# Kernel optimization log

Hardware: AMD Instinct MI355X
Metric: run time of the kernel (lower is better)

The kernel has to match this reference:

```python
import jax, jax.numpy as jnp
import numpy as np

# MSDeformAttn dims inferred from Linear shapes: 8 heads * 4 levels * 2 points
H, L, P, D, C = 8, 4, 2, 32, 256
SHAPES = [(128, 128), (64, 64), (32, 32), (16, 16)]  # (H_l, W_l) per level
NV = sum(h * w for h, w in SHAPES)  # 21760
STARTS = np.cumsum([0] + [h * w for h, w in SHAPES])


def _bilinear(val, lx, ly, Hl, Wl):
    """grid_sample(align_corners=False, padding='zeros') equivalent.
    val: [B, H, Hl*Wl, D]; lx, ly: [B, H, N] normalized sample coords in [0,1].
    Returns [B, H, N, D]."""
    x = lx * Wl - 0.5
    y = ly * Hl - 0.5
    x0 = jnp.floor(x)
    y0 = jnp.floor(y)
    fx = x - x0
    fy = y - y0
    x0i = x0.astype(jnp.int32)
    y0i = y0.astype(jnp.int32)
    out = jnp.zeros(val.shape[:2] + (x.shape[-1], val.shape[-1]), val.dtype)
    corners = ((0, 0, (1 - fx) * (1 - fy)), (1, 0, fx * (1 - fy)),
               (0, 1, (1 - fx) * fy), (1, 1, fx * fy))
    for dx, dy, w in corners:
        xi = x0i + dx
        yi = y0i + dy
        valid = ((xi >= 0) & (xi < Wl) & (yi >= 0) & (yi < Hl)).astype(val.dtype)
        idx = jnp.clip(yi, 0, Hl - 1) * Wl + jnp.clip(xi, 0, Wl - 1)
        g = jnp.take_along_axis(val, idx[..., None], axis=2)  # [B,H,N,D]
        out = out + g * (w * valid)[..., None]
    return out


def setup_inputs() -> dict:
    key = jax.random.key(0)
    ks = jax.random.split(key, 8)
    B, NQ = 4, 1000
    s = 0.02
    return {
        "query": jax.random.normal(ks[0], (B, NQ, C), jnp.float32),
        "value": jax.random.normal(ks[1], (B, NV, C), jnp.float32),
        "reference_points": jax.random.uniform(ks[2], (B, NQ, L, 2), jnp.float32),
        "W_off": jax.random.normal(ks[3], (C, H * L * P * 2), jnp.float32) * s,
        "b_off": jnp.zeros((H * L * P * 2,), jnp.float32),
        "W_attn": jax.random.normal(ks[4], (C, H * L * P), jnp.float32) * s,
        "b_attn": jnp.zeros((H * L * P,), jnp.float32),
        "W_val": jax.random.normal(ks[5], (C, C), jnp.float32) * s,
        "b_val": jnp.zeros((C,), jnp.float32),
        "W_out": jax.random.normal(ks[6], (C, C), jnp.float32) * s,
        "b_out": jnp.zeros((C,), jnp.float32),
    }


def reference(query, value, reference_points, W_off, b_off, W_attn, b_attn,
              W_val, b_val, W_out, b_out):
    B, NQ, _ = query.shape
    # value projection -> per-head values [B, H, NV, D]
    v = (value @ W_val + b_val).reshape(B, NV, H, D).transpose(0, 2, 1, 3)
    # sampling offsets [B, NQ, H, L, P, 2]
    off = (query @ W_off + b_off).reshape(B, NQ, H, L, P, 2)
    # attention weights: softmax over L*P
    attn = jax.nn.softmax((query @ W_attn + b_attn).reshape(B, NQ, H, L * P), axis=-1)
    attn = attn.reshape(B, NQ, H, L, P)
    # normalizer (W_l, H_l) per level, matching Deformable-DETR
    wh = jnp.asarray([[w, h] for h, w in SHAPES], dtype=query.dtype)  # [L,2]
    loc = reference_points[:, :, None, :, None, :] + off / wh[None, None, None, :, None, :]
    out = jnp.zeros((B, H, NQ, D), dtype=query.dtype)
    for l, (hl, wl) in enumerate(SHAPES):
        vl = v[:, :, STARTS[l]:STARTS[l + 1], :]                 # [B,H,hl*wl,D]
        lx = loc[:, :, :, l, :, 0].transpose(0, 2, 1, 3).reshape(B, H, NQ * P)
        ly = loc[:, :, :, l, :, 1].transpose(0, 2, 1, 3).reshape(B, H, NQ * P)
        s = _bilinear(vl, lx, ly, hl, wl).reshape(B, H, NQ, P, D)
        al = attn[:, :, :, l, :].transpose(0, 2, 1, 3)           # [B,H,NQ,P]
        out = out + jnp.sum(s * al[..., None], axis=3)
    out = out.transpose(0, 2, 1, 3).reshape(B, NQ, C)
    return out @ W_out + b_out  # dropout(p=0) is identity
```

## Files before the change

kernel.cpp:

```cpp
#include <hip/hip_runtime.h>

#define HH 8
#define LL 4
#define PP 2
#define DD 32
#define CC 256
#define NVV 21760
#define NQQ 1000
#define BB 4
#define NQT (BB * NQQ)

typedef __attribute__((ext_vector_type(8))) short short8;
typedef __attribute__((ext_vector_type(4))) short shortv4;
typedef __attribute__((ext_vector_type(4))) float f32x4;

__device__ __forceinline__ unsigned short f2bf(float f) {
    unsigned u = __float_as_uint(f);
    u += 0x7FFF + ((u >> 16) & 1);
    return (unsigned short)(u >> 16);
}
__device__ __forceinline__ float bf2f(unsigned short h) {
    return __uint_as_float(((unsigned)h) << 16);
}

__device__ __forceinline__ void gload_lds16(const void* g, void* l) {
    __builtin_amdgcn_global_load_lds(
        (const __attribute__((address_space(1))) unsigned int*)g,
        (__attribute__((address_space(3))) unsigned int*)l, 16, 0, 0);
}

__global__ __launch_bounds__(256) void prep_kernel(
    const float* __restrict__ Wv, const float* __restrict__ Woff,
    const float* __restrict__ Wattn, const float* __restrict__ Wout,
    unsigned short* __restrict__ Wslc, unsigned short* __restrict__ W1T,
    unsigned short* __restrict__ WoT)
{
    const int c = blockIdx.x;
    const int n = threadIdx.x;
    Wslc[(c >> 5) * 8192 + n * 32 + (c & 31)] = f2bf(Wv[c * CC + n]);
    if (n < 192) {
        float x = (n < 128) ? Woff[c * 128 + n] : Wattn[c * 64 + (n - 128)];
        W1T[n * CC + c] = f2bf(x);
    }
    WoT[n * CC + c] = f2bf(Wout[c * CC + n]);
}

__global__ __launch_bounds__(512) void valproj_mfma(
    const float* __restrict__ value, const unsigned short* __restrict__ Wslc,
    const float* __restrict__ bv, unsigned short* __restrict__ v_out)
{
    __shared__ __align__(16) unsigned short Bs[8][256][32];

    const int tid = threadIdx.x;
    const int w = tid >> 6;
    const int lane = tid & 63;
    const int lr = lane & 15;
    const int q = lane >> 4;
    const int bm = blockIdx.x * 128;
    const int b = bm / NVV;

#pragma unroll
    for (int i = 0; i < 16; ++i) {
        size_t off = (size_t)i * 8192 + (size_t)tid * 16;
        gload_lds16((const char*)Wslc + off, (char*)&Bs[0][0][0] + off);
    }
    __syncthreads();

    const float* arow = value + (size_t)(bm + w * 16 + lr) * CC;
    float4 a0[8], a1[8];
#pragma unroll
    for (int s = 0; s < 8; ++s) {
        const float* p = arow + s * 32 + q * 8;
        a0[s] = *(const float4*)p;
        a1[s] = *(const float4*)(p + 4);
    }

    f32x4 acc[16] = {};
#pragma unroll
    for (int s = 0; s < 8; ++s) {
        short8 af;
        af[0] = (short)f2bf(a0[s].x); af[1] = (short)f2bf(a0[s].y);
        af[2] = (short)f2bf(a0[s].z); af[3] = (short)f2bf(a0[s].w);
        af[4] = (short)f2bf(a1[s].x); af[5] = (short)f2bf(a1[s].y);
        af[6] = (short)f2bf(a1[s].z); af[7] = (short)f2bf(a1[s].w);
#pragma unroll
        for (int nf = 0; nf < 16; ++nf) {
            short8 bf = *(const short8*)&Bs[s][nf * 16 + lr][q * 8];
            acc[nf] = __builtin_amdgcn_mfma_f32_16x16x32_bf16(af, bf, acc[nf],
                                                              0, 0, 0);
        }
    }

#pragma unroll
    for (int nf = 0; nf < 16; ++nf) {
        int col = nf * 16 + lr;
        int h = col >> 5, d = col & 31;
        float bias = bv[col];
        int n0 = bm - b * NVV + w * 16 + q * 4;
        size_t obase = (size_t)((b * HH + h) * NVV + n0) * DD + d;
#pragma unroll
        for (int r = 0; r < 4; ++r)
            v_out[obase + (size_t)r * DD] = f2bf(acc[nf][r] + bias);
    }
}

__global__ __launch_bounds__(256) void logits_mfma(
    const float* __restrict__ query, const unsigned short* __restrict__ W1T,
    const float* __restrict__ b_off, const float* __restrict__ b_attn,
    float* __restrict__ logits)
{
    __shared__ unsigned short As[32][72];
    __shared__ unsigned short Bs[192][72];
    const int tid = threadIdx.x;
    const int lane = tid & 63;
    const int wave = tid >> 6;
    const int bm = blockIdx.x * 32;
    const int lr = lane & 15;
    const int q = lane >> 4;
    f32x4 acc[2][3] = {};

    for (int k0 = 0; k0 < CC; k0 += 64) {
        float4 a[2];
        short8 wv[6];
#pragma unroll
        for (int i = 0; i < 2; ++i) {
            int u = tid + 256 * i;
            a[i] = *(const float4*)&query[(size_t)(bm + (u >> 4)) * CC + k0 +
                                          (u & 15) * 4];
        }
#pragma unroll
        for (int i = 0; i < 6; ++i) {
            int u = tid + 256 * i;
            wv[i] = *(const short8*)&W1T[(size_t)(u >> 3) * CC + k0 + (u & 7) * 8];
        }
        __syncthreads();
#pragma unroll
        for (int i = 0; i < 2; ++i) {
            int u = tid + 256 * i;
            shortv4 p;
            p[0] = (short)f2bf(a[i].x); p[1] = (short)f2bf(a[i].y);
            p[2] = (short)f2bf(a[i].z); p[3] = (short)f2bf(a[i].w);
            *(shortv4*)&As[u >> 4][(u & 15) * 4] = p;
        }
#pragma unroll
        for (int i = 0; i < 6; ++i) {
            int u = tid + 256 * i;
            *(short8*)&Bs[u >> 3][(u & 7) * 8] = wv[i];
        }
        __syncthreads();

#pragma unroll
        for (int kk = 0; kk < 2; ++kk) {
            short8 afr[2], bfr[3];
#pragma unroll
            for (int mf = 0; mf < 2; ++mf)
                afr[mf] = *(const short8*)&As[mf * 16 + lr][kk * 32 + q * 8];
#pragma unroll
            for (int nf = 0; nf < 3; ++nf)
                bfr[nf] =
                    *(const short8*)&Bs[wave * 48 + nf * 16 + lr][kk * 32 + q * 8];
#pragma unroll
            for (int mf = 0; mf < 2; ++mf)
#pragma unroll
                for (int nf = 0; nf < 3; ++nf)
                    acc[mf][nf] = __builtin_amdgcn_mfma_f32_16x16x32_bf16(
                        afr[mf], bfr[nf], acc[mf][nf], 0, 0, 0);
        }
        __syncthreads();
    }

#pragma unroll
    for (int nf = 0; nf < 3; ++nf) {
        int col = wave * 48 + nf * 16 + lr;
        float bias = (col < 128) ? b_off[col] : b_attn[col - 128];
#pragma unroll
        for (int mf = 0; mf < 2; ++mf)
#pragma unroll
            for (int r = 0; r < 4; ++r) {
                int m = bm + mf * 16 + q * 4 + r;
                logits[(size_t)m * 192 + col] = acc[mf][nf][r] + bias;
            }
    }
}

__global__ __launch_bounds__(256) void sample_kernel(
    const float* __restrict__ logits,
    const float* __restrict__ refp,
    const unsigned short* __restrict__ v,
    unsigned short* __restrict__ mid)
{
    __shared__ float offl[128];
    __shared__ float attnl[64];
    __shared__ float refl[8];

    const int qy = blockIdx.x;
    const int b = qy / NQQ;
    const int tid = threadIdx.x;

    if (tid < 192) {
        float t = logits[(size_t)qy * 192 + tid];
        if (tid < 128) offl[tid] = t;
        else attnl[tid - 128] = t;
    } else if (tid < 200) {
        refl[tid - 192] = refp[(size_t)qy * 8 + (tid - 192)];
    }
    __syncthreads();

    if (tid < 8) {
        float m = -1e30f;
#pragma unroll
        for (int j = 0; j < 8; ++j) m = fmaxf(m, attnl[tid * 8 + j]);
        float s = 0.f, e[8];
#pragma unroll
        for (int j = 0; j < 8; ++j) {
            e[j] = __expf(attnl[tid * 8 + j] - m);
            s += e[j];
        }
        float inv = 1.f / s;
#pragma unroll
        for (int j = 0; j < 8; ++j) attnl[tid * 8 + j] = e[j] * inv;
    }
    __syncthreads();

    const int h = tid >> 5, d = tid & 31;
    const unsigned short* vh = v + (size_t)(b * HH + h) * NVV * DD;
    const int starts[4] = {0, 16384, 20480, 21504};
    const float szs[4] = {128.f, 64.f, 32.f, 16.f};

    float acc = 0.f;
#pragma unroll
    for (int l = 0; l < LL; ++l) {
        const float S = szs[l];
        const int Wl = (int)S;
        const float refx = refl[l * 2 + 0];
        const float refy = refl[l * 2 + 1];
        const unsigned short* vl = vh + (size_t)starts[l] * DD;
#pragma unroll
        for (int p = 0; p < PP; ++p) {
            const int oi = h * 16 + l * 4 + p * 2;
            float lx = refx + offl[oi + 0] / S;
            float ly = refy + offl[oi + 1] / S;
            float x = lx * S - 0.5f;
            float y = ly * S - 0.5f;
            float x0f = floorf(x), y0f = floorf(y);
            float fx = x - x0f, fy = y - y0f;
            int x0 = (int)x0f, y0 = (int)y0f;
            float a = attnl[h * 8 + l * 2 + p];
            float sacc = 0.f;
#pragma unroll
            for (int dy = 0; dy < 2; ++dy) {
#pragma unroll
                for (int dx = 0; dx < 2; ++dx) {
                    int xi = x0 + dx, yi = y0 + dy;
                    float wgt = (dx ? fx : 1.f - fx) * (dy ? fy : 1.f - fy);
                    bool valid = (xi >= 0) && (xi < Wl) && (yi >= 0) && (yi < Wl);
                    int xc = min(max(xi, 0), Wl - 1);
                    int yc = min(max(yi, 0), Wl - 1);
                    float g = bf2f(vl[(size_t)(yc * Wl + xc) * DD + d]);
                    sacc += g * (valid ? wgt : 0.f);
                }
            }
            acc += a * sacc;
        }
    }
    mid[(size_t)qy * CC + h * 32 + d] = f2bf(acc);
}

__global__ __launch_bounds__(256) void out_mfma(
    const unsigned short* __restrict__ mid,
    const unsigned short* __restrict__ WoT, const float* __restrict__ b_out,
    float* __restrict__ out)
{
    __shared__ unsigned short As[32][72];
    __shared__ unsigned short Bs[256][72];
    const int tid = threadIdx.x;
    const int lane = tid & 63;
    const int wave = tid >> 6;
    const int bm = blockIdx.x * 32;
    const int lr = lane & 15;
    const int q = lane >> 4;
    f32x4 acc[2][4] = {};

    for (int k0 = 0; k0 < CC; k0 += 64) {
        short8 a0 = *(const short8*)&mid[(size_t)(bm + (tid >> 3)) * CC + k0 +
                                         (tid & 7) * 8];
        short8 wv[8];
#pragma unroll
        for (int i = 0; i < 8; ++i) {
            int u = tid + 256 * i;
            wv[i] = *(const short8*)&WoT[(size_t)(u >> 3) * CC + k0 + (u & 7) * 8];
        }
        __syncthreads();
        *(short8*)&As[tid >> 3][(tid & 7) * 8] = a0;
#pragma unroll
        for (int i = 0; i < 8; ++i) {
            int u = tid + 256 * i;
            *(short8*)&Bs[u >> 3][(u & 7) * 8] = wv[i];
        }
        __syncthreads();

#pragma unroll
        for (int kk = 0; kk < 2; ++kk) {
            short8 afr[2], bfr[4];
#pragma unroll
            for (int mf = 0; mf < 2; ++mf)
                afr[mf] = *(const short8*)&As[mf * 16 + lr][kk * 32 + q * 8];
#pragma unroll
            for (int nf = 0; nf < 4; ++nf)
                bfr[nf] =
                    *(const short8*)&Bs[wave * 64 + nf * 16 + lr][kk * 32 + q * 8];
#pragma unroll
            for (int mf = 0; mf < 2; ++mf)
#pragma unroll
                for (int nf = 0; nf < 4; ++nf)
                    acc[mf][nf] = __builtin_amdgcn_mfma_f32_16x16x32_bf16(
                        afr[mf], bfr[nf], acc[mf][nf], 0, 0, 0);
        }
        __syncthreads();
    }

#pragma unroll
    for (int nf = 0; nf < 4; ++nf) {
        int col = wave * 64 + nf * 16 + lr;
        float bias = b_out[col];
#pragma unroll
        for (int mf = 0; mf < 2; ++mf)
#pragma unroll
            for (int r = 0; r < 4; ++r) {
                int m = bm + mf * 16 + q * 4 + r;
                out[(size_t)m * CC + col] = acc[mf][nf][r] + bias;
            }
    }
}

extern "C" void kernel_launch(void* const* d_in, const int* in_sizes, int n_in,
                              void* d_out, int out_size, void* d_ws, size_t ws_size,
                              hipStream_t stream) {
    const float* query  = (const float*)d_in[0];
    const float* value  = (const float*)d_in[1];
    const float* refp   = (const float*)d_in[2];
    const float* W_off  = (const float*)d_in[3];
    const float* b_off  = (const float*)d_in[4];
    const float* W_attn = (const float*)d_in[5];
    const float* b_attn = (const float*)d_in[6];
    const float* W_val  = (const float*)d_in[7];
    const float* b_val  = (const float*)d_in[8];
    const float* W_out  = (const float*)d_in[9];
    const float* b_out  = (const float*)d_in[10];
    float* out = (float*)d_out;

    char* ws = (char*)d_ws;
    unsigned short* Wslc   = (unsigned short*)(ws);
    unsigned short* v_ws   = (unsigned short*)(ws + 131072);
    unsigned short* W1T    = (unsigned short*)(ws + 44695552);
    unsigned short* WoT    = (unsigned short*)(ws + 44793856);
    float*          logits = (float*)(ws + 44924928);
    unsigned short* mid    = (unsigned short*)(ws + 47996928);

    prep_kernel<<<CC, 256, 0, stream>>>(W_val, W_off, W_attn, W_out,
                                        Wslc, W1T, WoT);
    valproj_mfma<<<(BB * NVV) / 128, 512, 0, stream>>>(value, Wslc, b_val, v_ws);
    logits_mfma<<<NQT / 32, 256, 0, stream>>>(query, W1T, b_off, b_attn, logits);
    sample_kernel<<<NQT, 256, 0, stream>>>(logits, refp, v_ws, mid);
    out_mfma<<<NQT / 32, 256, 0, stream>>>(mid, WoT, b_out, out);
}
```

Measured before the change: 68.15 us.

## Retile value projection into N-halves with swizzled LDS and coalesced row-major output

The value-projection GEMM is split into two N-halves per 128-row tile, with twice as many blocks, and uses a 2x2 wave layout. An XOR swizzle on the weight LDS layout avoids bank conflicts, A-tile loads are double-buffered, and the bf16 packing uses the hardware cvt_pk instruction. The output is staged through LDS and written row-major [B,NV,256] with 16-byte stores instead of scattered per-head 2-byte writes. The sampling kernel is changed to index this new layout, so each bilinear corner gather now strides 512 bytes per texel rather than 64.

```diff
diff --git a/kernel.cpp b/kernel.cpp
--- a/kernel.cpp
+++ b/kernel.cpp
@@ -22,6 +22,11 @@
 __device__ __forceinline__ float bf2f(unsigned short h) {
     return __uint_as_float(((unsigned)h) << 16);
 }
+__device__ __forceinline__ unsigned cvtpk(float lo, float hi) {
+    unsigned r;
+    asm volatile("v_cvt_pk_bf16_f32 %0, %1, %2" : "=v"(r) : "v"(lo), "v"(hi));
+    return r;
+}
 
 __device__ __forceinline__ void gload_lds16(const void* g, void* l) {
     __builtin_amdgcn_global_load_lds(
@@ -37,7 +42,12 @@
 {
     const int c = blockIdx.x;
     const int n = threadIdx.x;
-    Wslc[(c >> 5) * 8192 + n * 32 + (c & 31)] = f2bf(Wv[c * CC + n]);
+    {
+        int half = n >> 7, n7 = n & 127, s = c >> 5, kk = c & 31;
+        unsigned addr = n7 * 64 + kk * 2;
+        addr ^= ((n7 & 3) << 4);
+        Wslc[half * 32768 + s * 4096 + (addr >> 1)] = f2bf(Wv[c * CC + n]);
+    }
     if (n < 192) {
         float x = (n < 128) ? Woff[c * 128 + n] : Wattn[c * 64 + (n - 128)];
         W1T[n * CC + c] = f2bf(x);
@@ -45,62 +55,97 @@
     WoT[n * CC + c] = f2bf(Wout[c * CC + n]);
 }
 
-__global__ __launch_bounds__(512) void valproj_mfma(
+__global__ __launch_bounds__(512, 4) void valproj_mfma(
     const float* __restrict__ value, const unsigned short* __restrict__ Wslc,
     const float* __restrict__ bv, unsigned short* __restrict__ v_out)
 {
-    __shared__ __align__(16) unsigned short Bs[8][256][32];
+    __shared__ __align__(16) unsigned short Bs[32768];
 
     const int tid = threadIdx.x;
     const int w = tid >> 6;
     const int lane = tid & 63;
+    const int wm = w >> 1;
+    const int wn = w & 1;
     const int lr = lane & 15;
     const int q = lane >> 4;
-    const int bm = blockIdx.x * 128;
-    const int b = bm / NVV;
-
-#pragma unroll
-    for (int i = 0; i < 16; ++i) {
+    const int mt = blockIdx.x >> 1;
+    const int hf = blockIdx.x & 1;
+    const int bm = mt * 128;
+
+#pragma unroll
+    for (int i = 0; i < 8; ++i) {
         size_t off = (size_t)i * 8192 + (size_t)tid * 16;
-        gload_lds16((const char*)Wslc + off, (char*)&Bs[0][0][0] + off);
+        gload_lds16((const char*)Wslc + (size_t)hf * 65536 + off,
+                    (char*)&Bs[0] + off);
     }
     __syncthreads();
 
-    const float* arow = value + (size_t)(bm + w * 16 + lr) * CC;
-    float4 a0[8], a1[8];
+    const float* arow0 = value + (size_t)(bm + wm * 32 + lr) * CC;
+
+    float4 ab[2][2][2];
+#define LOADA(p, s)                                                          \
+    {                                                                        \
+        _Pragma("unroll") for (int mf = 0; mf < 2; ++mf) {                   \
+            const float* pp = arow0 + mf * 16 * CC + (s) * 32 + q * 8;       \
+            ab[p][mf][0] = *(const float4*)pp;                               \
+            ab[p][mf][1] = *(const float4*)(pp + 4);                         \
+        }                                                                    \
+    }
+
+    LOADA(0, 0);
+    LOADA(1, 1);
+
+    f32x4 acc[2][4] = {};
 #pragma unroll
     for (int s = 0; s < 8; ++s) {
-        const float* p = arow + s * 32 + q * 8;
-        a0[s] = *(const float4*)p;
-        a1[s] = *(const float4*)(p + 4);
-    }
-
-    f32x4 acc[16] = {};
-#pragma unroll
-    for (int s = 0; s < 8; ++s) {
-        short8 af;
-        af[0] = (short)f2bf(a0[s].x); af[1] = (short)f2bf(a0[s].y);
-        af[2] = (short)f2bf(a0[s].z); af[3] = (short)f2bf(a0[s].w);
-        af[4] = (short)f2bf(a1[s].x); af[5] = (short)f2bf(a1[s].y);
-        af[6] = (short)f2bf(a1[s].z); af[7] = (short)f2bf(a1[s].w);
-#pragma unroll
-        for (int nf = 0; nf < 16; ++nf) {
-            short8 bf = *(const short8*)&Bs[s][nf * 16 + lr][q * 8];
-            acc[nf] = __builtin_amdgcn_mfma_f32_16x16x32_bf16(af, bf, acc[nf],
-                                                              0, 0, 0);
-        }
-    }
-
-#pragma unroll
-    for (int nf = 0; nf < 16; ++nf) {
-        int col = nf * 16 + lr;
-        int h = col >> 5, d = col & 31;
-        float bias = bv[col];
-        int n0 = bm - b * NVV + w * 16 + q * 4;
-        size_t obase = (size_t)((b * HH + h) * NVV + n0) * DD + d;
-#pragma unroll
-        for (int r = 0; r < 4; ++r)
-            v_out[obase + (size_t)r * DD] = f2bf(acc[nf][r] + bias);
+        const int cur = s & 1;
+        short8 af[2];
+#pragma unroll
+        for (int mf = 0; mf < 2; ++mf) {
+            float4 f0 = ab[cur][mf][0], f1 = ab[cur][mf][1];
+            uint4 uv = {cvtpk(f0.x, f0.y), cvtpk(f0.z, f0.w),
+                        cvtpk(f1.x, f1.y), cvtpk(f1.z, f1.w)};
+            af[mf] = __builtin_bit_cast(short8, uv);
+        }
+        if (s < 6) LOADA(cur, s + 2);
+        short8 bfr[4];
+#pragma unroll
+        for (int nf = 0; nf < 4; ++nf) {
+            int idx = s * 4096 +
+                      (((wn * 64 + nf * 16 + lr) * 32 + q * 8) ^ ((lr & 3) << 3));
+            bfr[nf] = *(const short8*)&Bs[idx];
+        }
+#pragma unroll
+        for (int mf = 0; mf < 2; ++mf)
+#pragma unroll
+            for (int nf = 0; nf < 4; ++nf)
+                acc[mf][nf] = __builtin_amdgcn_mfma_f32_16x16x32_bf16(
+                    af[mf], bfr[nf], acc[mf][nf], 0, 0, 0);
+    }
+#undef LOADA
+
+    __syncthreads();
+#pragma unroll
+    for (int nf = 0; nf < 4; ++nf) {
+        int col = wn * 64 + nf * 16 + lr;
+        float bias = bv[hf * 128 + col];
+#pragma unroll
+        for (int mf = 0; mf < 2; ++mf)
+#pragma unroll
+            for (int r = 0; r < 4; ++r) {
+                int row = wm * 32 + mf * 16 + q * 4 + r;
+                Bs[row * 136 + col] = f2bf(acc[mf][nf][r] + bias);
+            }
+    }
+    __syncthreads();
+    {
+        int row = tid >> 2, ch = tid & 3;
+        size_t obase = (size_t)(bm + row) * 256 + hf * 128 + ch * 32;
+#pragma unroll
+        for (int i = 0; i < 4; ++i) {
+            short8 val = *(const short8*)&Bs[row * 136 + ch * 32 + i * 8];
+            *(short8*)&v_out[obase + i * 8] = val;
+        }
     }
 }
 
@@ -110,7 +155,7 @@
     float* __restrict__ logits)
 {
     __shared__ unsigned short As[32][72];
-    __shared__ unsigned short Bs[192][72];
+    __shared__ unsigned short Bsl[192][72];
     const int tid = threadIdx.x;
     const int lane = tid & 63;
     const int wave = tid >> 6;
@@ -145,7 +190,7 @@
 #pragma unroll
         for (int i = 0; i < 6; ++i) {
             int u = tid + 256 * i;
-            *(short8*)&Bs[u >> 3][(u & 7) * 8] = wv[i];
+            *(short8*)&Bsl[u >> 3][(u & 7) * 8] = wv[i];
         }
         __syncthreads();
 
@@ -158,7 +203,7 @@
 #pragma unroll
             for (int nf = 0; nf < 3; ++nf)
                 bfr[nf] =
-                    *(const short8*)&Bs[wave * 48 + nf * 16 + lr][kk * 32 + q * 8];
+                    *(const short8*)&Bsl[wave * 48 + nf * 16 + lr][kk * 32 + q * 8];
 #pragma unroll
             for (int mf = 0; mf < 2; ++mf)
 #pragma unroll
@@ -223,7 +268,6 @@
     __syncthreads();
 
     const int h = tid >> 5, d = tid & 31;
-    const unsigned short* vh = v + (size_t)(b * HH + h) * NVV * DD;
     const int starts[4] = {0, 16384, 20480, 21504};
     const float szs[4] = {128.f, 64.f, 32.f, 16.f};
 
@@ -234,7 +278,8 @@
         const int Wl = (int)S;
         const float refx = refl[l * 2 + 0];
         const float refy = refl[l * 2 + 1];
-        const unsigned short* vl = vh + (size_t)starts[l] * DD;
+        const unsigned short* vl =
+            v + (size_t)(b * NVV + starts[l]) * 256 + h * 32 + d;
 #pragma unroll
         for (int p = 0; p < PP; ++p) {
             const int oi = h * 16 + l * 4 + p * 2;
@@ -256,7 +301,7 @@
                     bool valid = (xi >= 0) && (xi < Wl) && (yi >= 0) && (yi < Wl);
                     int xc = min(max(xi, 0), Wl - 1);
                     int yc = min(max(yi, 0), Wl - 1);
-                    float g = bf2f(vl[(size_t)(yc * Wl + xc) * DD + d]);
+                    float g = bf2f(vl[(size_t)(yc * Wl + xc) * 256]);
                     sacc += g * (valid ? wgt : 0.f);
                 }
             }
@@ -272,7 +317,7 @@
     float* __restrict__ out)
 {
     __shared__ unsigned short As[32][72];
-    __shared__ unsigned short Bs[256][72];
+    __shared__ unsigned short Bso[256][72];
     const int tid = threadIdx.x;
     const int lane = tid & 63;
     const int wave = tid >> 6;
@@ -295,7 +340,7 @@
 #pragma unroll
         for (int i = 0; i < 8; ++i) {
             int u = tid + 256 * i;
-            *(short8*)&Bs[u >> 3][(u & 7) * 8] = wv[i];
+            *(short8*)&Bso[u >> 3][(u & 7) * 8] = wv[i];
         }
         __syncthreads();
 
@@ -308,7 +353,7 @@
 #pragma unroll
             for (int nf = 0; nf < 4; ++nf)
                 bfr[nf] =
-                    *(const short8*)&Bs[wave * 64 + nf * 16 + lr][kk * 32 + q * 8];
+                    *(const short8*)&Bso[wave * 64 + nf * 16 + lr][kk * 32 + q * 8];
 #pragma unroll
             for (int mf = 0; mf < 2; ++mf)
 #pragma unroll
@@ -359,7 +404,8 @@
 
     prep_kernel<<<CC, 256, 0, stream>>>(W_val, W_off, W_attn, W_out,
                                         Wslc, W1T, WoT);
-    valproj_mfma<<<(BB * NVV) / 128, 512, 0, stream>>>(value, Wslc, b_val, v_ws);
+    valproj_mfma<<<(BB * NVV) / 128 * 2, 512, 0, stream>>>(value, Wslc, b_val,
+                                                           v_ws);
     logits_mfma<<<NQT / 32, 256, 0, stream>>>(query, W1T, b_off, b_attn, logits);
     sample_kernel<<<NQT, 256, 0, stream>>>(logits, refp, v_ws, mid);
     out_mfma<<<NQT / 32, 256, 0, stream>>>(mid, WoT, b_out, out);
```

Result: slower. 95.36 us (+39.9%).

## Reorder value projection after sampling to skip full value-map projection

Applied to the files above, without the earlier changes.

Drops the projection of the whole value map (87k rows x 256 x 256). Since bilinear sampling and attention weighting are linear, it instead samples the raw fp32 value rows, aggregates them per query and head, and then applies the per-head slice of W_val to that aggregate, adding the bias scaled by the summed corner weights. This removes a large GEMM and its bf16 intermediate write. In exchange each sample gathers full 256-wide fp32 rows instead of 32-wide bf16 head slices, and each block runs a scalar, non-MFMA per-query projection from LDS.

```diff
diff --git a/kernel.cpp b/kernel.cpp
--- a/kernel.cpp
+++ b/kernel.cpp
@@ -9,6 +9,7 @@
 #define NQQ 1000
 #define BB 4
 #define NQT (BB * NQQ)
+#define QB 4
 
 typedef __attribute__((ext_vector_type(8))) short short8;
 typedef __attribute__((ext_vector_type(4))) short shortv4;
@@ -23,85 +24,20 @@
     return __uint_as_float(((unsigned)h) << 16);
 }
 
-__device__ __forceinline__ void gload_lds16(const void* g, void* l) {
-    __builtin_amdgcn_global_load_lds(
-        (const __attribute__((address_space(1))) unsigned int*)g,
-        (__attribute__((address_space(3))) unsigned int*)l, 16, 0, 0);
-}
-
 __global__ __launch_bounds__(256) void prep_kernel(
     const float* __restrict__ Wv, const float* __restrict__ Woff,
     const float* __restrict__ Wattn, const float* __restrict__ Wout,
-    unsigned short* __restrict__ Wslc, unsigned short* __restrict__ W1T,
+    unsigned short* __restrict__ WT, unsigned short* __restrict__ W1T,
     unsigned short* __restrict__ WoT)
 {
     const int c = blockIdx.x;
     const int n = threadIdx.x;
-    Wslc[(c >> 5) * 8192 + n * 32 + (c & 31)] = f2bf(Wv[c * CC + n]);
+    WT[n * CC + c] = f2bf(Wv[c * CC + n]);
     if (n < 192) {
         float x = (n < 128) ? Woff[c * 128 + n] : Wattn[c * 64 + (n - 128)];
         W1T[n * CC + c] = f2bf(x);
     }
     WoT[n * CC + c] = f2bf(Wout[c * CC + n]);
-}
-
-__global__ __launch_bounds__(512) void valproj_mfma(
-    const float* __restrict__ value, const unsigned short* __restrict__ Wslc,
-    const float* __restrict__ bv, unsigned short* __restrict__ v_out)
-{
-    __shared__ __align__(16) unsigned short Bs[8][256][32];
-
-    const int tid = threadIdx.x;
-    const int w = tid >> 6;
-    const int lane = tid & 63;
-    const int lr = lane & 15;
-    const int q = lane >> 4;
-    const int bm = blockIdx.x * 128;
-    const int b = bm / NVV;
-
-#pragma unroll
-    for (int i = 0; i < 16; ++i) {
-        size_t off = (size_t)i * 8192 + (size_t)tid * 16;
-        gload_lds16((const char*)Wslc + off, (char*)&Bs[0][0][0] + off);
-    }
-    __syncthreads();
-
-    const float* arow = value + (size_t)(bm + w * 16 + lr) * CC;
-    float4 a0[8], a1[8];
-#pragma unroll
-    for (int s = 0; s < 8; ++s) {
-        const float* p = arow + s * 32 + q * 8;
-        a0[s] = *(const float4*)p;
-        a1[s] = *(const float4*)(p + 4);
-    }
-
-    f32x4 acc[16] = {};
-#pragma unroll
-    for (int s = 0; s < 8; ++s) {
-        short8 af;
-        af[0] = (short)f2bf(a0[s].x); af[1] = (short)f2bf(a0[s].y);
-        af[2] = (short)f2bf(a0[s].z); af[3] = (short)f2bf(a0[s].w);
-        af[4] = (short)f2bf(a1[s].x); af[5] = (short)f2bf(a1[s].y);
-        af[6] = (short)f2bf(a1[s].z); af[7] = (short)f2bf(a1[s].w);
-#pragma unroll
-        for (int nf = 0; nf < 16; ++nf) {
-            short8 bf = *(const short8*)&Bs[s][nf * 16 + lr][q * 8];
-            acc[nf] = __builtin_amdgcn_mfma_f32_16x16x32_bf16(af, bf, acc[nf],
-                                                              0, 0, 0);
-        }
-    }
-
-#pragma unroll
-    for (int nf = 0; nf < 16; ++nf) {
-        int col = nf * 16 + lr;
-        int h = col >> 5, d = col & 31;
-        float bias = bv[col];
-        int n0 = bm - b * NVV + w * 16 + q * 4;
-        size_t obase = (size_t)((b * HH + h) * NVV + n0) * DD + d;
-#pragma unroll
-        for (int r = 0; r < 4; ++r)
-            v_out[obase + (size_t)r * DD] = f2bf(acc[nf][r] + bias);
-    }
 }
 
 __global__ __launch_bounds__(256) void logits_mfma(
@@ -110,7 +46,7 @@
     float* __restrict__ logits)
 {
     __shared__ unsigned short As[32][72];
-    __shared__ unsigned short Bs[192][72];
+    __shared__ unsigned short Bsl[192][72];
     const int tid = threadIdx.x;
     const int lane = tid & 63;
     const int wave = tid >> 6;
@@ -145,7 +81,7 @@
 #pragma unroll
         for (int i = 0; i < 6; ++i) {
             int u = tid + 256 * i;
-            *(short8*)&Bs[u >> 3][(u & 7) * 8] = wv[i];
+            *(short8*)&Bsl[u >> 3][(u & 7) * 8] = wv[i];
         }
         __syncthreads();
 
@@ -158,7 +94,7 @@
 #pragma unroll
             for (int nf = 0; nf < 3; ++nf)
                 bfr[nf] =
-                    *(const short8*)&Bs[wave * 48 + nf * 16 + lr][kk * 32 + q * 8];
+                    *(const short8*)&Bsl[wave * 48 + nf * 16 + lr][kk * 32 + q * 8];
 #pragma unroll
             for (int mf = 0; mf < 2; ++mf)
 #pragma unroll
@@ -183,87 +119,136 @@
     }
 }
 
-__global__ __launch_bounds__(256) void sample_kernel(
+__global__ __launch_bounds__(256) void sample_agg_proj(
     const float* __restrict__ logits,
     const float* __restrict__ refp,
-    const unsigned short* __restrict__ v,
+    const float* __restrict__ value,
+    const unsigned short* __restrict__ WT,
+    const float* __restrict__ b_val,
     unsigned short* __restrict__ mid)
 {
-    __shared__ float offl[128];
-    __shared__ float attnl[64];
-    __shared__ float refl[8];
-
-    const int qy = blockIdx.x;
-    const int b = qy / NQQ;
+    __shared__ float offl[QB][128];
+    __shared__ float attnl[QB][64];
+    __shared__ float refl[QB][8];
+    __shared__ float agg[QB * 8 * 256];
+    __shared__ float wsum[QB][8];
+
+    const int bq0 = blockIdx.x * QB;
+    const int b = bq0 / NQQ;
     const int tid = threadIdx.x;
-
-    if (tid < 192) {
-        float t = logits[(size_t)qy * 192 + tid];
-        if (tid < 128) offl[tid] = t;
-        else attnl[tid - 128] = t;
-    } else if (tid < 200) {
-        refl[tid - 192] = refp[(size_t)qy * 8 + (tid - 192)];
-    }
+    const int lane = tid & 63;
+    const int w = tid >> 6;
+
+#pragma unroll
+    for (int qi = 0; qi < QB; ++qi) {
+        if (tid < 192) {
+            float t = logits[(size_t)(bq0 + qi) * 192 + tid];
+            if (tid < 128) offl[qi][tid] = t;
+            else attnl[qi][tid - 128] = t;
+        }
+    }
+    if (tid < QB * 8) refl[tid >> 3][tid & 7] = refp[(size_t)bq0 * 8 + tid];
     __syncthreads();
 
-    if (tid < 8) {
+    if (tid < QB * 8) {
+        int qi = tid >> 3, h = tid & 7;
         float m = -1e30f;
 #pragma unroll
-        for (int j = 0; j < 8; ++j) m = fmaxf(m, attnl[tid * 8 + j]);
+        for (int j = 0; j < 8; ++j) m = fmaxf(m, attnl[qi][h * 8 + j]);
         float s = 0.f, e[8];
 #pragma unroll
         for (int j = 0; j < 8; ++j) {
-            e[j] = __expf(attnl[tid * 8 + j] - m);
+            e[j] = __expf(attnl[qi][h * 8 + j] - m);
             s += e[j];
         }
         float inv = 1.f / s;
 #pragma unroll
-        for (int j = 0; j < 8; ++j) attnl[tid * 8 + j] = e[j] * inv;
+        for (int j = 0; j < 8; ++j) attnl[qi][h * 8 + j] = e[j] * inv;
     }
     __syncthreads();
 
-    const int h = tid >> 5, d = tid & 31;
-    const unsigned short* vh = v + (size_t)(b * HH + h) * NVV * DD;
     const int starts[4] = {0, 16384, 20480, 21504};
     const float szs[4] = {128.f, 64.f, 32.f, 16.f};
 
-    float acc = 0.f;
-#pragma unroll
-    for (int l = 0; l < LL; ++l) {
-        const float S = szs[l];
-        const int Wl = (int)S;
-        const float refx = refl[l * 2 + 0];
-        const float refy = refl[l * 2 + 1];
-        const unsigned short* vl = vh + (size_t)starts[l] * DD;
-#pragma unroll
-        for (int p = 0; p < PP; ++p) {
-            const int oi = h * 16 + l * 4 + p * 2;
-            float lx = refx + offl[oi + 0] / S;
-            float ly = refy + offl[oi + 1] / S;
-            float x = lx * S - 0.5f;
-            float y = ly * S - 0.5f;
-            float x0f = floorf(x), y0f = floorf(y);
-            float fx = x - x0f, fy = y - y0f;
-            int x0 = (int)x0f, y0 = (int)y0f;
-            float a = attnl[h * 8 + l * 2 + p];
-            float sacc = 0.f;
-#pragma unroll
-            for (int dy = 0; dy < 2; ++dy) {
-#pragma unroll
-                for (int dx = 0; dx < 2; ++dx) {
-                    int xi = x0 + dx, yi = y0 + dy;
-                    float wgt = (dx ? fx : 1.f - fx) * (dy ? fy : 1.f - fy);
-                    bool valid = (xi >= 0) && (xi < Wl) && (yi >= 0) && (yi < Wl);
-                    int xc = min(max(xi, 0), Wl - 1);
-                    int yc = min(max(yi, 0), Wl - 1);
-                    float g = bf2f(vl[(size_t)(yc * Wl + xc) * DD + d]);
-                    sacc += g * (valid ? wgt : 0.f);
+#pragma unroll
+    for (int qi = 0; qi < QB; ++qi) {
+#pragma unroll
+        for (int hh = 0; hh < 2; ++hh) {
+            const int h = w + hh * 4;
+            f32x4 acc = {0.f, 0.f, 0.f, 0.f};
+            float ws = 0.f;
+#pragma unroll
+            for (int l = 0; l < LL; ++l) {
+                const float S = szs[l];
+                const int Wl = (int)S;
+                const float refx = refl[qi][l * 2 + 0];
+                const float refy = refl[qi][l * 2 + 1];
+                const float* vbase =
+                    value + (size_t)(b * NVV + starts[l]) * 256 + (lane << 2);
+#pragma unroll
+                for (int p = 0; p < PP; ++p) {
+                    const int oi = h * 16 + l * 4 + p * 2;
+                    float lx = refx + offl[qi][oi + 0] / S;
+                    float ly = refy + offl[qi][oi + 1] / S;
+                    float x = lx * S - 0.5f;
+                    float y = ly * S - 0.5f;
+                    float x0f = floorf(x), y0f = floorf(y);
+                    float fx = x - x0f, fy = y - y0f;
+                    int x0 = (int)x0f, y0 = (int)y0f;
+                    float a = attnl[qi][h * 8 + l * 2 + p];
+#pragma unroll
+                    for (int dy = 0; dy < 2; ++dy) {
+#pragma unroll
+                        for (int dx = 0; dx < 2; ++dx) {
+                            int xi = x0 + dx, yi = y0 + dy;
+                            float wgt =
+                                (dx ? fx : 1.f - fx) * (dy ? fy : 1.f - fy);
+                            bool valid = (xi >= 0) && (xi < Wl) &&
+                                         (yi >= 0) && (yi < Wl);
+                            int xc = min(max(xi, 0), Wl - 1);
+                            int yc = min(max(yi, 0), Wl - 1);
+                            float cw = valid ? a * wgt : 0.f;
+                            f32x4 g = *(const f32x4*)(vbase +
+                                                      (size_t)(yc * Wl + xc) *
+                                                          256);
+                            acc[0] += cw * g[0];
+                            acc[1] += cw * g[1];
+                            acc[2] += cw * g[2];
+                            acc[3] += cw * g[3];
+                            ws += cw;
+                        }
+                    }
                 }
             }
-            acc += a * sacc;
-        }
-    }
-    mid[(size_t)qy * CC + h * 32 + d] = f2bf(acc);
+            *(f32x4*)&agg[((qi << 3) + h) * 256 + (lane << 2)] = acc;
+            if (lane == 0) wsum[qi][h] = ws;
+        }
+    }
+    __syncthreads();
+
+    {
+        const int n = tid;
+        const int h = n >> 5;
+        const unsigned short* wrow = WT + (size_t)n * CC;
+        float accm[QB] = {0.f, 0.f, 0.f, 0.f};
+#pragma unroll 4
+        for (int c0 = 0; c0 < CC; c0 += 8) {
+            short8 wv8 = *(const short8*)&wrow[c0];
+#pragma unroll
+            for (int j = 0; j < 8; ++j) {
+                float wv = bf2f((unsigned short)wv8[j]);
+                int c = c0 + j;
+#pragma unroll
+                for (int qi = 0; qi < QB; ++qi)
+                    accm[qi] += agg[((qi << 3) + h) * 256 + c] * wv;
+            }
+        }
+        float bn = b_val[n];
+#pragma unroll
+        for (int qi = 0; qi < QB; ++qi)
+            mid[(size_t)(bq0 + qi) * CC + n] =
+                f2bf(accm[qi] + wsum[qi][h] * bn);
+    }
 }
 
 __global__ __launch_bounds__(256) void out_mfma(
@@ -272,7 +257,7 @@
     float* __restrict__ out)
 {
     __shared__ unsigned short As[32][72];
-    __shared__ unsigned short Bs[256][72];
+    __shared__ unsigned short Bso[256][72];
     const int tid = threadIdx.x;
     const int lane = tid & 63;
     const int wave = tid >> 6;
@@ -295,7 +280,7 @@
 #pragma unroll
         for (int i = 0; i < 8; ++i) {
             int u = tid + 256 * i;
-            *(short8*)&Bs[u >> 3][(u & 7) * 8] = wv[i];
+            *(short8*)&Bso[u >> 3][(u & 7) * 8] = wv[i];
         }
         __syncthreads();
 
@@ -308,7 +293,7 @@
 #pragma unroll
             for (int nf = 0; nf < 4; ++nf)
                 bfr[nf] =
-                    *(const short8*)&Bs[wave * 64 + nf * 16 + lr][kk * 32 + q * 8];
+                    *(const short8*)&Bso[wave * 64 + nf * 16 + lr][kk * 32 + q * 8];
 #pragma unroll
             for (int mf = 0; mf < 2; ++mf)
 #pragma unroll
@@ -350,17 +335,16 @@
     float* out = (float*)d_out;
 
     char* ws = (char*)d_ws;
-    unsigned short* Wslc   = (unsigned short*)(ws);
-    unsigned short* v_ws   = (unsigned short*)(ws + 131072);
-    unsigned short* W1T    = (unsigned short*)(ws + 44695552);
-    unsigned short* WoT    = (unsigned short*)(ws + 44793856);
-    float*          logits = (float*)(ws + 44924928);
-    unsigned short* mid    = (unsigned short*)(ws + 47996928);
+    unsigned short* WT     = (unsigned short*)(ws);
+    unsigned short* W1T    = (unsigned short*)(ws + 131072);
+    unsigned short* WoT    = (unsigned short*)(ws + 262144);
+    float*          logits = (float*)(ws + 393216);
+    unsigned short* mid    = (unsigned short*)(ws + 3465216);
 
     prep_kernel<<<CC, 256, 0, stream>>>(W_val, W_off, W_attn, W_out,
-                                        Wslc, W1T, WoT);
-    valproj_mfma<<<(BB * NVV) / 128, 512, 0, stream>>>(value, Wslc, b_val, v_ws);
+                                        WT, W1T, WoT);
     logits_mfma<<<NQT / 32, 256, 0, stream>>>(query, W1T, b_off, b_attn, logits);
-    sample_kernel<<<NQT, 256, 0, stream>>>(logits, refp, v_ws, mid);
+    sample_agg_proj<<<NQT / QB, 256, 0, stream>>>(logits, refp, value, WT,
+                                                  b_val, mid);
     out_mfma<<<NQT / 32, 256, 0, stream>>>(mid, WoT, b_out, out);
 }
```

After: 86.15 us. 26.4% more time.
